# Kernel optimization log

Hardware: AMD Instinct MI355X
Metric: run time of the kernel (lower is better)

Reference implementation:

```python
import jax, jax.numpy as jnp
import numpy as np

N_NODES = 50000
N_EDGES = 800000
IN_CH = 128
OUT_CH = 64
HEADS = 4
NEG_SLOPE = 0.2


def setup_inputs() -> dict:
    key = jax.random.key(0)
    k1, k2, k3, k4, k5 = jax.random.split(key, 5)
    x = jax.random.normal(k1, (N_NODES, IN_CH), dtype=jnp.float32)
    edge_index = jax.random.randint(k2, (2, N_EDGES), 0, N_NODES, dtype=jnp.int64)
    # Glorot-ish scaled params
    W = jax.random.normal(k3, (IN_CH, HEADS * OUT_CH), dtype=jnp.float32) * (1.0 / np.sqrt(IN_CH))
    att_src = jax.random.normal(k4, (HEADS, OUT_CH), dtype=jnp.float32) * (1.0 / np.sqrt(OUT_CH))
    att_dst = jax.random.normal(k5, (HEADS, OUT_CH), dtype=jnp.float32) * (1.0 / np.sqrt(OUT_CH))
    bias = jnp.zeros((HEADS * OUT_CH,), dtype=jnp.float32)
    return {"x": x, "edge_index": edge_index, "W": W, "att_src": att_src, "att_dst": att_dst, "bias": bias}


def reference(x, edge_index, W, att_src, att_dst, bias):
    N = x.shape[0]
    H, C = att_src.shape
    # PyG GATConv default add_self_loops=True
    loops = jnp.arange(N, dtype=edge_index.dtype)
    src = jnp.concatenate([edge_index[0], loops])  # message source j
    dst = jnp.concatenate([edge_index[1], loops])  # message target i
    # Linear transform per head: [N, H, C]
    h = (x @ W).reshape(N, H, C)
    # Per-node attention logits: [N, H]
    a_src = jnp.sum(h * att_src[None], axis=-1)
    a_dst = jnp.sum(h * att_dst[None], axis=-1)
    # Per-edge raw score (alpha_src from source node, alpha_dst from target node)
    e = jax.nn.leaky_relu(a_src[src] + a_dst[dst], NEG_SLOPE)  # [E, H]
    # Segment-softmax over incoming edges of each target node
    m = jax.ops.segment_max(e, dst, num_segments=N)  # [N, H]
    m = jnp.where(jnp.isfinite(m), m, 0.0)  # nodes with no edges -> 0
    ex = jnp.exp(e - m[dst])
    denom = jax.ops.segment_sum(ex, dst, num_segments=N)  # [N, H]
    alpha = ex / (denom[dst] + 1e-16)  # [E, H]
    # Weighted aggregate of source features: [N, H, C]
    msg = h[src] * alpha[:, :, None]
    out = jax.ops.segment_sum(msg, dst, num_segments=N)
    # concat=True: flatten heads, add bias
    return out.reshape(N, H * C) + bias
```

## Files before the change

### kernel.cpp

```cpp
#include <hip/hip_runtime.h>

#define N_NODES 50000
#define N_EDGES 800000
#define IN_CH 128
#define OUT_CH 64
#define HEADS 4
#define HC 256
#define NEG_SLOPE 0.2f
#define GEMM_BLOCKS 782
#define COUNT_BLOCKS 782

#define HB_OFF       0UL
#define WSW_OFF      25600000UL
#define ASRC_OFF     25665536UL
#define ADST_OFF     26465536UL
#define COUNTS_OFF   27265536UL
#define OFFSETS_OFF  27465536UL
#define CURSOR_OFF   27665536UL
#define BSUMS_OFF    27865536UL
#define CSR_OFF      27866560UL
#define EXV_OFF      31066560UL

typedef __attribute__((ext_vector_type(8))) short short8;
typedef __attribute__((ext_vector_type(4))) float f32x4;

__device__ __forceinline__ unsigned short f2bf(float f) {
  unsigned int u = __float_as_uint(f);
  unsigned int r = (u + 0x7fffu + ((u >> 16) & 1u)) >> 16;
  return (unsigned short)r;
}
__device__ __forceinline__ float bf2f_lo(unsigned int u) {
  return __uint_as_float(u << 16);
}
__device__ __forceinline__ float bf2f_hi(unsigned int u) {
  return __uint_as_float(u & 0xffff0000u);
}
__device__ __forceinline__ float lrelu(float e) {
  return e > 0.f ? e : NEG_SLOPE * e;
}

__global__ __launch_bounds__(256) void swizzle_W(const float* __restrict__ W,
                                                 unsigned short* __restrict__ Wsw) {
  int idx = blockIdx.x * 256 + threadIdx.x;
  if (idx >= 4096) return;
  int l = idx & 63;
  int kc = (idx >> 6) & 3;
  int t = idx >> 8;
  int kbase = kc * 32 + (l >> 4) * 8;
  int col = t * 16 + (l & 15);
  unsigned int p[4];
#pragma unroll
  for (int j = 0; j < 4; ++j) {
    unsigned int lo = f2bf(W[(size_t)(kbase + 2 * j) * HC + col]);
    unsigned int hi = f2bf(W[(size_t)(kbase + 2 * j + 1) * HC + col]);
    p[j] = lo | (hi << 16);
  }
  *(uint4*)(Wsw + (size_t)idx * 8) = make_uint4(p[0], p[1], p[2], p[3]);
}

__global__ __launch_bounds__(256) void gemm_count(const float* __restrict__ x,
                                                  const unsigned short* __restrict__ Wsw,
                                                  const float* __restrict__ att_s,
                                                  const float* __restrict__ att_d,
                                                  const int* __restrict__ dstv,
                                                  unsigned short* __restrict__ hb,
                                                  float* __restrict__ a_src,
                                                  float* __restrict__ a_dst,
                                                  int* __restrict__ counts) {
  __shared__ float Cs[4][16][256];

  if (blockIdx.x >= GEMM_BLOCKS) {
    int base = (blockIdx.x - GEMM_BLOCKS) * 1024 + threadIdx.x;
#pragma unroll
    for (int k = 0; k < 4; ++k) {
      int e = base + k * 256;
      if (e < N_EDGES) atomicAdd(&counts[dstv[e]], 1);
    }
    return;
  }

  const int wave = threadIdx.x >> 6;
  const int l = threadIdx.x & 63;
  const int q = l >> 4;
  const int m = l & 15;
  const int mrow = blockIdx.x * 64 + wave * 16 + m;
  const bool mvalid = mrow < N_NODES;
  const int rc = mvalid ? mrow : (N_NODES - 1);

  short8 a[4];
  const float* xr = x + (size_t)rc * IN_CH + q * 8;
#pragma unroll
  for (int kc = 0; kc < 4; ++kc) {
    float4 u = *(const float4*)(xr + kc * 32);
    float4 v = *(const float4*)(xr + kc * 32 + 4);
    short8 t;
    t[0] = (short)f2bf(u.x); t[1] = (short)f2bf(u.y);
    t[2] = (short)f2bf(u.z); t[3] = (short)f2bf(u.w);
    t[4] = (short)f2bf(v.x); t[5] = (short)f2bf(v.y);
    t[6] = (short)f2bf(v.z); t[7] = (short)f2bf(v.w);
    a[kc] = t;
  }

#pragma unroll
  for (int t = 0; t < 16; ++t) {
    f32x4 acc = {0.f, 0.f, 0.f, 0.f};
#pragma unroll
    for (int kc = 0; kc < 4; ++kc) {
      short8 b = *(const short8*)(Wsw + ((size_t)(t * 4 + kc) * 64 + l) * 8);
      acc = __builtin_amdgcn_mfma_f32_16x16x32_bf16(a[kc], b, acc, 0, 0, 0);
    }
#pragma unroll
    for (int r = 0; r < 4; ++r) {
      int row = q * 4 + r;
      Cs[wave][row][(t * 16 + m) ^ (row << 2)] = acc[r];
    }
  }
  __syncthreads();

  float as = 0.f, ad = 0.f;
  unsigned short* hrow = hb + (size_t)mrow * HC + q * 64;
  const int sw = m << 2;
#pragma unroll
  for (int i = 0; i < 8; ++i) {
    int col0 = q * 64 + i * 8;
    float4 c1 = *(const float4*)&Cs[wave][m][(col0) ^ sw];
    float4 c2 = *(const float4*)&Cs[wave][m][(col0 + 4) ^ sw];
    float4 s1 = *(const float4*)(att_s + col0);
    float4 s2 = *(const float4*)(att_s + col0 + 4);
    float4 d1 = *(const float4*)(att_d + col0);
    float4 d2 = *(const float4*)(att_d + col0 + 4);
    as += c1.x * s1.x + c1.y * s1.y + c1.z * s1.z + c1.w * s1.w;
    as += c2.x * s2.x + c2.y * s2.y + c2.z * s2.z + c2.w * s2.w;
    ad += c1.x * d1.x + c1.y * d1.y + c1.z * d1.z + c1.w * d1.w;
    ad += c2.x * d2.x + c2.y * d2.y + c2.z * d2.z + c2.w * d2.w;
    if (mvalid) {
      uint4 p;
      p.x = (unsigned int)f2bf(c1.x) | ((unsigned int)f2bf(c1.y) << 16);
      p.y = (unsigned int)f2bf(c1.z) | ((unsigned int)f2bf(c1.w) << 16);
      p.z = (unsigned int)f2bf(c2.x) | ((unsigned int)f2bf(c2.y) << 16);
      p.w = (unsigned int)f2bf(c2.z) | ((unsigned int)f2bf(c2.w) << 16);
      *(uint4*)(hrow + i * 8) = p;
    }
  }
  if (mvalid) {
    a_src[mrow * HEADS + q] = as;
    a_dst[mrow * HEADS + q] = ad;
  }
}

__global__ __launch_bounds__(256) void scan1(const int* __restrict__ counts,
                                             int* __restrict__ offsets,
                                             int* __restrict__ bsums) {
  __shared__ int sd[256];
  const int base = blockIdx.x * 1024;
  const int t = threadIdx.x;
  int v[4];
  int tsum = 0;
#pragma unroll
  for (int k = 0; k < 4; ++k) {
    int i = base + t * 4 + k;
    v[k] = (i < N_NODES) ? counts[i] : 0;
    tsum += v[k];
  }
  sd[t] = tsum;
  __syncthreads();
  for (int off = 1; off < 256; off <<= 1) {
    int xval = (t >= off) ? sd[t - off] : 0;
    __syncthreads();
    sd[t] += xval;
    __syncthreads();
  }
  int excl = sd[t] - tsum;
  int run = excl;
#pragma unroll
  for (int k = 0; k < 4; ++k) {
    int i = base + t * 4 + k;
    if (i < N_NODES) offsets[i] = run;
    run += v[k];
  }
  if (t == 255) bsums[blockIdx.x] = sd[255];
}

__global__ void scan2(int* __restrict__ bsums, int nb) {
  if (threadIdx.x == 0 && blockIdx.x == 0) {
    int run = 0;
    for (int b = 0; b < nb; ++b) {
      int t = bsums[b];
      bsums[b] = run;
      run += t;
    }
  }
}

__global__ __launch_bounds__(256) void scan3(int* __restrict__ offsets,
                                             const int* __restrict__ bsums,
                                             int* __restrict__ cursor) {
  const int base = blockIdx.x * 1024;
  const int t = threadIdx.x;
  int add = bsums[blockIdx.x];
#pragma unroll
  for (int k = 0; k < 4; ++k) {
    int i = base + t * 4 + k;
    if (i < N_NODES) {
      int o = offsets[i] + add;
      offsets[i] = o;
      cursor[i] = o;
    }
  }
}

__global__ __launch_bounds__(256) void scatter_k(const int* __restrict__ src,
                                                 const int* __restrict__ dst,
                                                 const float* __restrict__ a_src,
                                                 const float* __restrict__ a_dst,
                                                 int* __restrict__ cursor,
                                                 int* __restrict__ csr,
                                                 float* __restrict__ exv) {
  int e = blockIdx.x * 256 + threadIdx.x;
  if (e < N_EDGES) {
    int s = src[e];
    int d = dst[e];
    float4 as = *(const float4*)(a_src + s * 4);
    float4 ad = *(const float4*)(a_dst + d * 4);
    float4 ex;
    ex.x = __expf(lrelu(as.x + ad.x));
    ex.y = __expf(lrelu(as.y + ad.y));
    ex.z = __expf(lrelu(as.z + ad.z));
    ex.w = __expf(lrelu(as.w + ad.w));
    int pos = atomicAdd(&cursor[d], 1);
    csr[pos] = s;
    *(float4*)(exv + (size_t)pos * 4) = ex;
  }
}

__global__ __launch_bounds__(256) void aggregate(const unsigned short* __restrict__ hb,
                                                 const float* __restrict__ a_src,
                                                 const float* __restrict__ a_dst,
                                                 const int* __restrict__ counts,
                                                 const int* __restrict__ offsets,
                                                 const int* __restrict__ csr,
                                                 const float* __restrict__ exv,
                                                 const float* __restrict__ bias,
                                                 float* __restrict__ out) {
  const int node = blockIdx.x * 4 + (threadIdx.x >> 6);
  const int l = threadIdx.x & 63;
  const int g = l >> 5;
  const int q = l & 31;
  const int hd = q >> 3;
  const int c0 = q * 8;
  const int deg = counts[node];
  const int start = offsets[node];

  float denom = 0.f;
  float acc[8] = {0.f, 0.f, 0.f, 0.f, 0.f, 0.f, 0.f, 0.f};
#pragma unroll 2
  for (int j = 0; j + g < deg; j += 2) {
    int idx = start + j + g;
    int s = csr[idx];
    float ex = exv[(size_t)idx * 4 + hd];
    uint4 hv = *(const uint4*)(hb + (size_t)s * HC + c0);
    denom += ex;
    acc[0] += bf2f_lo(hv.x) * ex;
    acc[1] += bf2f_hi(hv.x) * ex;
    acc[2] += bf2f_lo(hv.y) * ex;
    acc[3] += bf2f_hi(hv.y) * ex;
    acc[4] += bf2f_lo(hv.z) * ex;
    acc[5] += bf2f_hi(hv.z) * ex;
    acc[6] += bf2f_lo(hv.w) * ex;
    acc[7] += bf2f_hi(hv.w) * ex;
  }
  denom += __shfl_xor(denom, 32);
#pragma unroll
  for (int k = 0; k < 8; ++k) acc[k] += __shfl_xor(acc[k], 32);

  float es = a_src[node * HEADS + hd] + a_dst[node * HEADS + hd];
  float ex_self = __expf(lrelu(es));
  denom += ex_self;
  uint4 hs = *(const uint4*)(hb + (size_t)node * HC + c0);
  acc[0] += bf2f_lo(hs.x) * ex_self;
  acc[1] += bf2f_hi(hs.x) * ex_self;
  acc[2] += bf2f_lo(hs.y) * ex_self;
  acc[3] += bf2f_hi(hs.y) * ex_self;
  acc[4] += bf2f_lo(hs.z) * ex_self;
  acc[5] += bf2f_hi(hs.z) * ex_self;
  acc[6] += bf2f_lo(hs.w) * ex_self;
  acc[7] += bf2f_hi(hs.w) * ex_self;

  if (g == 0) {
    float inv = 1.f / (denom + 1e-16f);
    float4 b1 = *(const float4*)(bias + c0);
    float4 b2 = *(const float4*)(bias + c0 + 4);
    float4 o1 = make_float4(acc[0] * inv + b1.x, acc[1] * inv + b1.y,
                            acc[2] * inv + b1.z, acc[3] * inv + b1.w);
    float4 o2 = make_float4(acc[4] * inv + b2.x, acc[5] * inv + b2.y,
                            acc[6] * inv + b2.z, acc[7] * inv + b2.w);
    *(float4*)(out + (size_t)node * HC + c0) = o1;
    *(float4*)(out + (size_t)node * HC + c0 + 4) = o2;
  }
}

extern "C" void kernel_launch(void* const* d_in, const int* in_sizes, int n_in,
                              void* d_out, int out_size, void* d_ws, size_t ws_size,
                              hipStream_t stream) {
  const float* x     = (const float*)d_in[0];
  const int*   ei    = (const int*)d_in[1];
  const float* W     = (const float*)d_in[2];
  const float* att_s = (const float*)d_in[3];
  const float* att_d = (const float*)d_in[4];
  const float* bias  = (const float*)d_in[5];
  float* out = (float*)d_out;

  char* ws = (char*)d_ws;
  unsigned short* hb  = (unsigned short*)(ws + HB_OFF);
  unsigned short* Wsw = (unsigned short*)(ws + WSW_OFF);
  float* a_src  = (float*)(ws + ASRC_OFF);
  float* a_dst  = (float*)(ws + ADST_OFF);
  int* counts   = (int*)(ws + COUNTS_OFF);
  int* offsets  = (int*)(ws + OFFSETS_OFF);
  int* cursor   = (int*)(ws + CURSOR_OFF);
  int* bsums    = (int*)(ws + BSUMS_OFF);
  int* csr      = (int*)(ws + CSR_OFF);
  float* exv    = (float*)(ws + EXV_OFF);

  const int* src = ei;
  const int* dst = ei + N_EDGES;

  hipMemsetAsync(counts, 0, N_NODES * sizeof(int), stream);

  swizzle_W<<<16, 256, 0, stream>>>(W, Wsw);
  gemm_count<<<GEMM_BLOCKS + COUNT_BLOCKS, 256, 0, stream>>>(
      x, Wsw, att_s, att_d, dst, hb, a_src, a_dst, counts);
  scan1<<<49, 256, 0, stream>>>(counts, offsets, bsums);
  scan2<<<1, 64, 0, stream>>>(bsums, 49);
  scan3<<<49, 256, 0, stream>>>(offsets, bsums, cursor);
  scatter_k<<<3125, 256, 0, stream>>>(src, dst, a_src, a_dst, cursor, csr, exv);
  aggregate<<<12500, 256, 0, stream>>>(hb, a_src, a_dst, counts, offsets, csr, exv, bias, out);
}
```

Measured before the change: 263.6 us.

## Fuse setup kernels, pack CSR records, widen aggregate to 4 edge groups

The memset is folded into the W swizzle kernel, and scan2/scan3 are merged into one kernel that scans the block sums with a wavefront. This removes two launches. The separate csr and exv arrays become a single 32-byte record per edge holding the source index and the four exp values. The aggregate kernel now processes 4 edges in parallel per wavefront, with each lane covering 16 channels, and a two-step shuffle reduction feeds a store from every lane. The aims are fewer launches, better memory coalescing, and more gather parallelism, at the cost of more registers and padded record traffic.

```diff
diff --git a/kernel.cpp b/kernel.cpp
--- a/kernel.cpp
+++ b/kernel.cpp
@@ -9,6 +9,7 @@
 #define NEG_SLOPE 0.2f
 #define GEMM_BLOCKS 782
 #define COUNT_BLOCKS 782
+#define SCAN_BLOCKS 49
 
 #define HB_OFF       0UL
 #define WSW_OFF      25600000UL
@@ -18,8 +19,7 @@
 #define OFFSETS_OFF  27465536UL
 #define CURSOR_OFF   27665536UL
 #define BSUMS_OFF    27865536UL
-#define CSR_OFF      27866560UL
-#define EXV_OFF      31066560UL
+#define REC_OFF      27866560UL
 
 typedef __attribute__((ext_vector_type(8))) short short8;
 typedef __attribute__((ext_vector_type(4))) float f32x4;
@@ -39,23 +39,28 @@
   return e > 0.f ? e : NEG_SLOPE * e;
 }
 
-__global__ __launch_bounds__(256) void swizzle_W(const float* __restrict__ W,
-                                                 unsigned short* __restrict__ Wsw) {
-  int idx = blockIdx.x * 256 + threadIdx.x;
-  if (idx >= 4096) return;
-  int l = idx & 63;
-  int kc = (idx >> 6) & 3;
-  int t = idx >> 8;
-  int kbase = kc * 32 + (l >> 4) * 8;
-  int col = t * 16 + (l & 15);
-  unsigned int p[4];
-#pragma unroll
-  for (int j = 0; j < 4; ++j) {
-    unsigned int lo = f2bf(W[(size_t)(kbase + 2 * j) * HC + col]);
-    unsigned int hi = f2bf(W[(size_t)(kbase + 2 * j + 1) * HC + col]);
-    p[j] = lo | (hi << 16);
-  }
-  *(uint4*)(Wsw + (size_t)idx * 8) = make_uint4(p[0], p[1], p[2], p[3]);
+__global__ __launch_bounds__(256) void init_k(const float* __restrict__ W,
+                                              unsigned short* __restrict__ Wsw,
+                                              int* __restrict__ counts) {
+  if (blockIdx.x < 16) {
+    int idx = blockIdx.x * 256 + threadIdx.x;
+    int l = idx & 63;
+    int kc = (idx >> 6) & 3;
+    int t = idx >> 8;
+    int kbase = kc * 32 + (l >> 4) * 8;
+    int col = t * 16 + (l & 15);
+    unsigned int p[4];
+#pragma unroll
+    for (int j = 0; j < 4; ++j) {
+      unsigned int lo = f2bf(W[(size_t)(kbase + 2 * j) * HC + col]);
+      unsigned int hi = f2bf(W[(size_t)(kbase + 2 * j + 1) * HC + col]);
+      p[j] = lo | (hi << 16);
+    }
+    *(uint4*)(Wsw + (size_t)idx * 8) = make_uint4(p[0], p[1], p[2], p[3]);
+  } else {
+    int i = (blockIdx.x - 16) * 256 + threadIdx.x;
+    if (i < N_NODES) counts[i] = 0;
+  }
 }
 
 __global__ __launch_bounds__(256) void gemm_count(const float* __restrict__ x,
@@ -181,23 +186,26 @@
   if (t == 255) bsums[blockIdx.x] = sd[255];
 }
 
-__global__ void scan2(int* __restrict__ bsums, int nb) {
-  if (threadIdx.x == 0 && blockIdx.x == 0) {
-    int run = 0;
-    for (int b = 0; b < nb; ++b) {
-      int t = bsums[b];
-      bsums[b] = run;
-      run += t;
-    }
-  }
-}
-
-__global__ __launch_bounds__(256) void scan3(int* __restrict__ offsets,
-                                             const int* __restrict__ bsums,
-                                             int* __restrict__ cursor) {
+__global__ __launch_bounds__(256) void scan23(int* __restrict__ offsets,
+                                              const int* __restrict__ bsums,
+                                              int* __restrict__ cursor) {
+  __shared__ int s_add;
+  if (threadIdx.x < 64) {
+    int lane = threadIdx.x;
+    int v = (lane < SCAN_BLOCKS) ? bsums[lane] : 0;
+#pragma unroll
+    for (int o = 1; o < 64; o <<= 1) {
+      int t = __shfl_up(v, o);
+      if (lane >= o) v += t;
+    }
+    int b = blockIdx.x;
+    int pre = (b == 0) ? 0 : __shfl(v, b - 1);
+    if (lane == 0) s_add = pre;
+  }
+  __syncthreads();
+  const int add = s_add;
   const int base = blockIdx.x * 1024;
   const int t = threadIdx.x;
-  int add = bsums[blockIdx.x];
 #pragma unroll
   for (int k = 0; k < 4; ++k) {
     int i = base + t * 4 + k;
@@ -214,8 +222,7 @@
                                                  const float* __restrict__ a_src,
                                                  const float* __restrict__ a_dst,
                                                  int* __restrict__ cursor,
-                                                 int* __restrict__ csr,
-                                                 float* __restrict__ exv) {
+                                                 char* __restrict__ rec) {
   int e = blockIdx.x * 256 + threadIdx.x;
   if (e < N_EDGES) {
     int s = src[e];
@@ -228,8 +235,10 @@
     ex.z = __expf(lrelu(as.z + ad.z));
     ex.w = __expf(lrelu(as.w + ad.w));
     int pos = atomicAdd(&cursor[d], 1);
-    csr[pos] = s;
-    *(float4*)(exv + (size_t)pos * 4) = ex;
+    char* rp = rec + (size_t)pos * 32;
+    *(uint4*)rp = make_uint4((unsigned)s, __float_as_uint(ex.x),
+                             __float_as_uint(ex.y), __float_as_uint(ex.z));
+    *(unsigned*)(rp + 16) = __float_as_uint(ex.w);
   }
 }
 
@@ -238,65 +247,73 @@
                                                  const float* __restrict__ a_dst,
                                                  const int* __restrict__ counts,
                                                  const int* __restrict__ offsets,
-                                                 const int* __restrict__ csr,
-                                                 const float* __restrict__ exv,
+                                                 const char* __restrict__ rec,
                                                  const float* __restrict__ bias,
                                                  float* __restrict__ out) {
   const int node = blockIdx.x * 4 + (threadIdx.x >> 6);
   const int l = threadIdx.x & 63;
-  const int g = l >> 5;
-  const int q = l & 31;
-  const int hd = q >> 3;
-  const int c0 = q * 8;
+  const int g = l >> 4;
+  const int q = l & 15;
+  const int hd = q >> 2;
+  const int cb = q * 32;
   const int deg = counts[node];
   const int start = offsets[node];
+  const char* hbase = (const char*)hb;
 
   float denom = 0.f;
-  float acc[8] = {0.f, 0.f, 0.f, 0.f, 0.f, 0.f, 0.f, 0.f};
+  float acc[16];
+#pragma unroll
+  for (int k = 0; k < 16; ++k) acc[k] = 0.f;
+
 #pragma unroll 2
-  for (int j = 0; j + g < deg; j += 2) {
+  for (int j = 0; j + g < deg; j += 4) {
     int idx = start + j + g;
-    int s = csr[idx];
-    float ex = exv[(size_t)idx * 4 + hd];
-    uint4 hv = *(const uint4*)(hb + (size_t)s * HC + c0);
+    const char* rp = rec + (size_t)idx * 32;
+    int s = *(const int*)rp;
+    float ex = *(const float*)(rp + 4 + hd * 4);
+    const char* hp = hbase + (size_t)s * 512 + cb;
+    uint4 h0 = *(const uint4*)hp;
+    uint4 h1 = *(const uint4*)(hp + 16);
     denom += ex;
-    acc[0] += bf2f_lo(hv.x) * ex;
-    acc[1] += bf2f_hi(hv.x) * ex;
-    acc[2] += bf2f_lo(hv.y) * ex;
-    acc[3] += bf2f_hi(hv.y) * ex;
-    acc[4] += bf2f_lo(hv.z) * ex;
-    acc[5] += bf2f_hi(hv.z) * ex;
-    acc[6] += bf2f_lo(hv.w) * ex;
-    acc[7] += bf2f_hi(hv.w) * ex;
-  }
+    acc[0] += bf2f_lo(h0.x) * ex;  acc[1] += bf2f_hi(h0.x) * ex;
+    acc[2] += bf2f_lo(h0.y) * ex;  acc[3] += bf2f_hi(h0.y) * ex;
+    acc[4] += bf2f_lo(h0.z) * ex;  acc[5] += bf2f_hi(h0.z) * ex;
+    acc[6] += bf2f_lo(h0.w) * ex;  acc[7] += bf2f_hi(h0.w) * ex;
+    acc[8] += bf2f_lo(h1.x) * ex;  acc[9] += bf2f_hi(h1.x) * ex;
+    acc[10] += bf2f_lo(h1.y) * ex; acc[11] += bf2f_hi(h1.y) * ex;
+    acc[12] += bf2f_lo(h1.z) * ex; acc[13] += bf2f_hi(h1.z) * ex;
+    acc[14] += bf2f_lo(h1.w) * ex; acc[15] += bf2f_hi(h1.w) * ex;
+  }
+
+  denom += __shfl_xor(denom, 16);
   denom += __shfl_xor(denom, 32);
 #pragma unroll
-  for (int k = 0; k < 8; ++k) acc[k] += __shfl_xor(acc[k], 32);
+  for (int k = 0; k < 16; ++k) {
+    acc[k] += __shfl_xor(acc[k], 16);
+    acc[k] += __shfl_xor(acc[k], 32);
+  }
 
   float es = a_src[node * HEADS + hd] + a_dst[node * HEADS + hd];
-  float ex_self = __expf(lrelu(es));
-  denom += ex_self;
-  uint4 hs = *(const uint4*)(hb + (size_t)node * HC + c0);
-  acc[0] += bf2f_lo(hs.x) * ex_self;
-  acc[1] += bf2f_hi(hs.x) * ex_self;
-  acc[2] += bf2f_lo(hs.y) * ex_self;
-  acc[3] += bf2f_hi(hs.y) * ex_self;
-  acc[4] += bf2f_lo(hs.z) * ex_self;
-  acc[5] += bf2f_hi(hs.z) * ex_self;
-  acc[6] += bf2f_lo(hs.w) * ex_self;
-  acc[7] += bf2f_hi(hs.w) * ex_self;
-
-  if (g == 0) {
-    float inv = 1.f / (denom + 1e-16f);
-    float4 b1 = *(const float4*)(bias + c0);
-    float4 b2 = *(const float4*)(bias + c0 + 4);
-    float4 o1 = make_float4(acc[0] * inv + b1.x, acc[1] * inv + b1.y,
-                            acc[2] * inv + b1.z, acc[3] * inv + b1.w);
-    float4 o2 = make_float4(acc[4] * inv + b2.x, acc[5] * inv + b2.y,
-                            acc[6] * inv + b2.z, acc[7] * inv + b2.w);
-    *(float4*)(out + (size_t)node * HC + c0) = o1;
-    *(float4*)(out + (size_t)node * HC + c0 + 4) = o2;
-  }
+  float exs = __expf(lrelu(es));
+  denom += exs;
+  const char* hp = hbase + (size_t)node * 512 + cb;
+  uint4 h0 = *(const uint4*)hp;
+  uint4 h1 = *(const uint4*)(hp + 16);
+  acc[0] += bf2f_lo(h0.x) * exs;  acc[1] += bf2f_hi(h0.x) * exs;
+  acc[2] += bf2f_lo(h0.y) * exs;  acc[3] += bf2f_hi(h0.y) * exs;
+  acc[4] += bf2f_lo(h0.z) * exs;  acc[5] += bf2f_hi(h0.z) * exs;
+  acc[6] += bf2f_lo(h0.w) * exs;  acc[7] += bf2f_hi(h0.w) * exs;
+  acc[8] += bf2f_lo(h1.x) * exs;  acc[9] += bf2f_hi(h1.x) * exs;
+  acc[10] += bf2f_lo(h1.y) * exs; acc[11] += bf2f_hi(h1.y) * exs;
+  acc[12] += bf2f_lo(h1.z) * exs; acc[13] += bf2f_hi(h1.z) * exs;
+  acc[14] += bf2f_lo(h1.w) * exs; acc[15] += bf2f_hi(h1.w) * exs;
+
+  float inv = 1.f / (denom + 1e-16f);
+  int c = q * 16 + g * 4;
+  float4 bv = *(const float4*)(bias + c);
+  float4 o = make_float4(acc[g * 4 + 0] * inv + bv.x, acc[g * 4 + 1] * inv + bv.y,
+                         acc[g * 4 + 2] * inv + bv.z, acc[g * 4 + 3] * inv + bv.w);
+  *(float4*)(out + (size_t)node * HC + c) = o;
 }
 
 extern "C" void kernel_launch(void* const* d_in, const int* in_sizes, int n_in,
@@ -319,20 +336,16 @@
   int* offsets  = (int*)(ws + OFFSETS_OFF);
   int* cursor   = (int*)(ws + CURSOR_OFF);
   int* bsums    = (int*)(ws + BSUMS_OFF);
-  int* csr      = (int*)(ws + CSR_OFF);
-  float* exv    = (float*)(ws + EXV_OFF);
+  char* rec     = (char*)(ws + REC_OFF);
 
   const int* src = ei;
   const int* dst = ei + N_EDGES;
 
-  hipMemsetAsync(counts, 0, N_NODES * sizeof(int), stream);
-
-  swizzle_W<<<16, 256, 0, stream>>>(W, Wsw);
+  init_k<<<16 + 196, 256, 0, stream>>>(W, Wsw, counts);
   gemm_count<<<GEMM_BLOCKS + COUNT_BLOCKS, 256, 0, stream>>>(
       x, Wsw, att_s, att_d, dst, hb, a_src, a_dst, counts);
-  scan1<<<49, 256, 0, stream>>>(counts, offsets, bsums);
-  scan2<<<1, 64, 0, stream>>>(bsums, 49);
-  scan3<<<49, 256, 0, stream>>>(offsets, bsums, cursor);
-  scatter_k<<<3125, 256, 0, stream>>>(src, dst, a_src, a_dst, cursor, csr, exv);
-  aggregate<<<12500, 256, 0, stream>>>(hb, a_src, a_dst, counts, offsets, csr, exv, bias, out);
-}
+  scan1<<<SCAN_BLOCKS, 256, 0, stream>>>(counts, offsets, bsums);
+  scan23<<<SCAN_BLOCKS, 256, 0, stream>>>(offsets, bsums, cursor);
+  scatter_k<<<3125, 256, 0, stream>>>(src, dst, a_src, a_dst, cursor, rec);
+  aggregate<<<12500, 256, 0, stream>>>(hb, a_src, a_dst, counts, offsets, rec, bias, out);
+}
```

Result: faster. 248.7 us (-5.6%).

## Fold attention vectors into W, fuse GEMM with scatter, pack edge records

Applied to the files above, without the earlier changes.

Attention logits are now computed straight from x using precomputed W·att vectors, so the GEMM no longer has to produce them. That lets the bf16 GEMM run in the same launch as the edge scatter, with LDS halved by processing columns in two chunks. The separate memset, swizzle and scan2 launches are merged into an init kernel and a fused scan23. CSR indices and exp weights are packed into 32-byte records so the aggregate reads one record per edge, and its unroll goes from 2 to 4. The trade-off is a second read of x and logits computed in fp32 from the folded weights, which differ slightly from the bf16-derived values.

```diff
diff --git a/kernel.cpp b/kernel.cpp
--- a/kernel.cpp
+++ b/kernel.cpp
@@ -7,8 +7,11 @@
 #define HEADS 4
 #define HC 256
 #define NEG_SLOPE 0.2f
+#define LOGIT_BLOCKS 3125
+#define CNT_BLOCKS 782
 #define GEMM_BLOCKS 782
-#define COUNT_BLOCKS 782
+#define SCAT_BLOCKS 3125
+#define SCAN_BLOCKS 49
 
 #define HB_OFF       0UL
 #define WSW_OFF      25600000UL
@@ -18,8 +21,9 @@
 #define OFFSETS_OFF  27465536UL
 #define CURSOR_OFF   27665536UL
 #define BSUMS_OFF    27865536UL
-#define CSR_OFF      27866560UL
-#define EXV_OFF      31066560UL
+#define WSV_OFF      27866560UL
+#define WDV_OFF      27868608UL
+#define REC_OFF      27870656UL
 
 typedef __attribute__((ext_vector_type(8))) short short8;
 typedef __attribute__((ext_vector_type(4))) float f32x4;
@@ -39,43 +43,185 @@
   return e > 0.f ? e : NEG_SLOPE * e;
 }
 
-__global__ __launch_bounds__(256) void swizzle_W(const float* __restrict__ W,
-                                                 unsigned short* __restrict__ Wsw) {
-  int idx = blockIdx.x * 256 + threadIdx.x;
-  if (idx >= 4096) return;
-  int l = idx & 63;
-  int kc = (idx >> 6) & 3;
-  int t = idx >> 8;
-  int kbase = kc * 32 + (l >> 4) * 8;
-  int col = t * 16 + (l & 15);
-  unsigned int p[4];
-#pragma unroll
-  for (int j = 0; j < 4; ++j) {
-    unsigned int lo = f2bf(W[(size_t)(kbase + 2 * j) * HC + col]);
-    unsigned int hi = f2bf(W[(size_t)(kbase + 2 * j + 1) * HC + col]);
-    p[j] = lo | (hi << 16);
-  }
-  *(uint4*)(Wsw + (size_t)idx * 8) = make_uint4(p[0], p[1], p[2], p[3]);
-}
-
-__global__ __launch_bounds__(256) void gemm_count(const float* __restrict__ x,
-                                                  const unsigned short* __restrict__ Wsw,
-                                                  const float* __restrict__ att_s,
-                                                  const float* __restrict__ att_d,
-                                                  const int* __restrict__ dstv,
-                                                  unsigned short* __restrict__ hb,
-                                                  float* __restrict__ a_src,
-                                                  float* __restrict__ a_dst,
-                                                  int* __restrict__ counts) {
-  __shared__ float Cs[4][16][256];
-
-  if (blockIdx.x >= GEMM_BLOCKS) {
-    int base = (blockIdx.x - GEMM_BLOCKS) * 1024 + threadIdx.x;
+__global__ __launch_bounds__(256) void init_k(const float* __restrict__ W,
+                                              const float* __restrict__ att_s,
+                                              const float* __restrict__ att_d,
+                                              unsigned short* __restrict__ Wsw,
+                                              float* __restrict__ wsv,
+                                              float* __restrict__ wdv,
+                                              int* __restrict__ counts) {
+  if (blockIdx.x < 16) {
+    int idx = blockIdx.x * 256 + threadIdx.x;
+    int l = idx & 63;
+    int kc = (idx >> 6) & 3;
+    int t = idx >> 8;
+    int kbase = kc * 32 + (l >> 4) * 8;
+    int col = t * 16 + (l & 15);
+    unsigned int p[4];
+#pragma unroll
+    for (int j = 0; j < 4; ++j) {
+      unsigned int lo = f2bf(W[(size_t)(kbase + 2 * j) * HC + col]);
+      unsigned int hi = f2bf(W[(size_t)(kbase + 2 * j + 1) * HC + col]);
+      p[j] = lo | (hi << 16);
+    }
+    *(uint4*)(Wsw + (size_t)idx * 8) = make_uint4(p[0], p[1], p[2], p[3]);
+  } else if (blockIdx.x == 16) {
+    int t = threadIdx.x;
+    int k = t >> 1;
+    int side = t & 1;
+    const float* att = side ? att_d : att_s;
+    float v[4] = {0.f, 0.f, 0.f, 0.f};
+    const float* wr = W + (size_t)k * HC;
+    for (int c = 0; c < 64; ++c) {
+#pragma unroll
+      for (int hd = 0; hd < 4; ++hd) v[hd] = fmaf(wr[hd * 64 + c], att[hd * 64 + c], v[hd]);
+    }
+    float* dp = side ? wdv : wsv;
+    *(float4*)(dp + k * 4) = make_float4(v[0], v[1], v[2], v[3]);
+  } else {
+    int i = (blockIdx.x - 17) * 256 + threadIdx.x;
+    if (i < N_NODES) counts[i] = 0;
+  }
+}
+
+__global__ __launch_bounds__(256) void logits_count(const float* __restrict__ x,
+                                                    const float* __restrict__ wsv,
+                                                    const float* __restrict__ wdv,
+                                                    const int* __restrict__ dstv,
+                                                    float* __restrict__ a_src,
+                                                    float* __restrict__ a_dst,
+                                                    int* __restrict__ counts) {
+  if (blockIdx.x >= LOGIT_BLOCKS) {
+    int base = (blockIdx.x - LOGIT_BLOCKS) * 1024 + threadIdx.x;
 #pragma unroll
     for (int k = 0; k < 4; ++k) {
       int e = base + k * 256;
       if (e < N_EDGES) atomicAdd(&counts[dstv[e]], 1);
     }
+    return;
+  }
+  const int t = threadIdx.x;
+  const int nl = t >> 4;
+  const int lane = t & 15;
+  const int node = blockIdx.x * 16 + nl;
+  const float* xr = x + (size_t)node * IN_CH + lane * 8;
+  float4 x0 = *(const float4*)xr;
+  float4 x1 = *(const float4*)(xr + 4);
+  float xs[8] = {x0.x, x0.y, x0.z, x0.w, x1.x, x1.y, x1.z, x1.w};
+  float as[4] = {0.f, 0.f, 0.f, 0.f}, ad[4] = {0.f, 0.f, 0.f, 0.f};
+#pragma unroll
+  for (int j = 0; j < 8; ++j) {
+    int k = lane * 8 + j;
+    float4 wv = *(const float4*)(wsv + k * 4);
+    float4 dv = *(const float4*)(wdv + k * 4);
+    as[0] = fmaf(xs[j], wv.x, as[0]); as[1] = fmaf(xs[j], wv.y, as[1]);
+    as[2] = fmaf(xs[j], wv.z, as[2]); as[3] = fmaf(xs[j], wv.w, as[3]);
+    ad[0] = fmaf(xs[j], dv.x, ad[0]); ad[1] = fmaf(xs[j], dv.y, ad[1]);
+    ad[2] = fmaf(xs[j], dv.z, ad[2]); ad[3] = fmaf(xs[j], dv.w, ad[3]);
+  }
+#pragma unroll
+  for (int mask = 1; mask < 16; mask <<= 1) {
+#pragma unroll
+    for (int hd = 0; hd < 4; ++hd) {
+      as[hd] += __shfl_xor(as[hd], mask);
+      ad[hd] += __shfl_xor(ad[hd], mask);
+    }
+  }
+  if (lane == 0) *(float4*)(a_src + node * 4) = make_float4(as[0], as[1], as[2], as[3]);
+  if (lane == 1) *(float4*)(a_dst + node * 4) = make_float4(ad[0], ad[1], ad[2], ad[3]);
+}
+
+__global__ __launch_bounds__(256) void scan1(const int* __restrict__ counts,
+                                             int* __restrict__ offsets,
+                                             int* __restrict__ bsums) {
+  __shared__ int sd[256];
+  const int base = blockIdx.x * 1024;
+  const int t = threadIdx.x;
+  int v[4];
+  int tsum = 0;
+#pragma unroll
+  for (int k = 0; k < 4; ++k) {
+    int i = base + t * 4 + k;
+    v[k] = (i < N_NODES) ? counts[i] : 0;
+    tsum += v[k];
+  }
+  sd[t] = tsum;
+  __syncthreads();
+  for (int off = 1; off < 256; off <<= 1) {
+    int xval = (t >= off) ? sd[t - off] : 0;
+    __syncthreads();
+    sd[t] += xval;
+    __syncthreads();
+  }
+  int excl = sd[t] - tsum;
+  int run = excl;
+#pragma unroll
+  for (int k = 0; k < 4; ++k) {
+    int i = base + t * 4 + k;
+    if (i < N_NODES) offsets[i] = run;
+    run += v[k];
+  }
+  if (t == 255) bsums[blockIdx.x] = sd[255];
+}
+
+__global__ __launch_bounds__(256) void scan23(int* __restrict__ offsets,
+                                              const int* __restrict__ bsums,
+                                              int* __restrict__ cursor) {
+  __shared__ int s_add;
+  if (threadIdx.x < 64) {
+    int lane = threadIdx.x;
+    int v = (lane < SCAN_BLOCKS) ? bsums[lane] : 0;
+#pragma unroll
+    for (int o = 1; o < 64; o <<= 1) {
+      int t = __shfl_up(v, o);
+      if (lane >= o) v += t;
+    }
+    int b = blockIdx.x;
+    int pre = (b == 0) ? 0 : __shfl(v, b - 1);
+    if (lane == 0) s_add = pre;
+  }
+  __syncthreads();
+  const int add = s_add;
+  const int base = blockIdx.x * 1024;
+  const int t = threadIdx.x;
+#pragma unroll
+  for (int k = 0; k < 4; ++k) {
+    int i = base + t * 4 + k;
+    if (i < N_NODES) {
+      int o = offsets[i] + add;
+      offsets[i] = o;
+      cursor[i] = o;
+    }
+  }
+}
+
+__global__ __launch_bounds__(256) void gemm_scatter(const float* __restrict__ x,
+                                                    const unsigned short* __restrict__ Wsw,
+                                                    const int* __restrict__ srcv,
+                                                    const int* __restrict__ dstv,
+                                                    const float* __restrict__ a_src,
+                                                    const float* __restrict__ a_dst,
+                                                    int* __restrict__ cursor,
+                                                    char* __restrict__ rec,
+                                                    unsigned short* __restrict__ hb) {
+  __shared__ float Cs[4][16][128];
+
+  if (blockIdx.x >= GEMM_BLOCKS) {
+    int e = (blockIdx.x - GEMM_BLOCKS) * 256 + threadIdx.x;
+    int s = srcv[e];
+    int d = dstv[e];
+    float4 as = *(const float4*)(a_src + s * 4);
+    float4 ad = *(const float4*)(a_dst + d * 4);
+    float4 ex;
+    ex.x = __expf(lrelu(as.x + ad.x));
+    ex.y = __expf(lrelu(as.y + ad.y));
+    ex.z = __expf(lrelu(as.z + ad.z));
+    ex.w = __expf(lrelu(as.w + ad.w));
+    int pos = atomicAdd(&cursor[d], 1);
+    char* rp = rec + (size_t)pos * 32;
+    *(uint4*)rp = make_uint4((unsigned)s, __float_as_uint(ex.x),
+                             __float_as_uint(ex.y), __float_as_uint(ex.z));
+    *(unsigned*)(rp + 16) = __float_as_uint(ex.w);
     return;
   }
 
@@ -101,135 +247,40 @@
     a[kc] = t;
   }
 
-#pragma unroll
-  for (int t = 0; t < 16; ++t) {
-    f32x4 acc = {0.f, 0.f, 0.f, 0.f};
-#pragma unroll
-    for (int kc = 0; kc < 4; ++kc) {
-      short8 b = *(const short8*)(Wsw + ((size_t)(t * 4 + kc) * 64 + l) * 8);
-      acc = __builtin_amdgcn_mfma_f32_16x16x32_bf16(a[kc], b, acc, 0, 0, 0);
-    }
-#pragma unroll
-    for (int r = 0; r < 4; ++r) {
-      int row = q * 4 + r;
-      Cs[wave][row][(t * 16 + m) ^ (row << 2)] = acc[r];
-    }
-  }
-  __syncthreads();
-
-  float as = 0.f, ad = 0.f;
   unsigned short* hrow = hb + (size_t)mrow * HC + q * 64;
   const int sw = m << 2;
 #pragma unroll
-  for (int i = 0; i < 8; ++i) {
-    int col0 = q * 64 + i * 8;
-    float4 c1 = *(const float4*)&Cs[wave][m][(col0) ^ sw];
-    float4 c2 = *(const float4*)&Cs[wave][m][(col0 + 4) ^ sw];
-    float4 s1 = *(const float4*)(att_s + col0);
-    float4 s2 = *(const float4*)(att_s + col0 + 4);
-    float4 d1 = *(const float4*)(att_d + col0);
-    float4 d2 = *(const float4*)(att_d + col0 + 4);
-    as += c1.x * s1.x + c1.y * s1.y + c1.z * s1.z + c1.w * s1.w;
-    as += c2.x * s2.x + c2.y * s2.y + c2.z * s2.z + c2.w * s2.w;
-    ad += c1.x * d1.x + c1.y * d1.y + c1.z * d1.z + c1.w * d1.w;
-    ad += c2.x * d2.x + c2.y * d2.y + c2.z * d2.z + c2.w * d2.w;
-    if (mvalid) {
-      uint4 p;
-      p.x = (unsigned int)f2bf(c1.x) | ((unsigned int)f2bf(c1.y) << 16);
-      p.y = (unsigned int)f2bf(c1.z) | ((unsigned int)f2bf(c1.w) << 16);
-      p.z = (unsigned int)f2bf(c2.x) | ((unsigned int)f2bf(c2.y) << 16);
-      p.w = (unsigned int)f2bf(c2.z) | ((unsigned int)f2bf(c2.w) << 16);
-      *(uint4*)(hrow + i * 8) = p;
-    }
-  }
-  if (mvalid) {
-    a_src[mrow * HEADS + q] = as;
-    a_dst[mrow * HEADS + q] = ad;
-  }
-}
-
-__global__ __launch_bounds__(256) void scan1(const int* __restrict__ counts,
-                                             int* __restrict__ offsets,
-                                             int* __restrict__ bsums) {
-  __shared__ int sd[256];
-  const int base = blockIdx.x * 1024;
-  const int t = threadIdx.x;
-  int v[4];
-  int tsum = 0;
-#pragma unroll
-  for (int k = 0; k < 4; ++k) {
-    int i = base + t * 4 + k;
-    v[k] = (i < N_NODES) ? counts[i] : 0;
-    tsum += v[k];
-  }
-  sd[t] = tsum;
-  __syncthreads();
-  for (int off = 1; off < 256; off <<= 1) {
-    int xval = (t >= off) ? sd[t - off] : 0;
-    __syncthreads();
-    sd[t] += xval;
-    __syncthreads();
-  }
-  int excl = sd[t] - tsum;
-  int run = excl;
-#pragma unroll
-  for (int k = 0; k < 4; ++k) {
-    int i = base + t * 4 + k;
-    if (i < N_NODES) offsets[i] = run;
-    run += v[k];
-  }
-  if (t == 255) bsums[blockIdx.x] = sd[255];
-}
-
-__global__ void scan2(int* __restrict__ bsums, int nb) {
-  if (threadIdx.x == 0 && blockIdx.x == 0) {
-    int run = 0;
-    for (int b = 0; b < nb; ++b) {
-      int t = bsums[b];
-      bsums[b] = run;
-      run += t;
-    }
-  }
-}
-
-__global__ __launch_bounds__(256) void scan3(int* __restrict__ offsets,
-                                             const int* __restrict__ bsums,
-                                             int* __restrict__ cursor) {
-  const int base = blockIdx.x * 1024;
-  const int t = threadIdx.x;
-  int add = bsums[blockIdx.x];
-#pragma unroll
-  for (int k = 0; k < 4; ++k) {
-    int i = base + t * 4 + k;
-    if (i < N_NODES) {
-      int o = offsets[i] + add;
-      offsets[i] = o;
-      cursor[i] = o;
-    }
-  }
-}
-
-__global__ __launch_bounds__(256) void scatter_k(const int* __restrict__ src,
-                                                 const int* __restrict__ dst,
-                                                 const float* __restrict__ a_src,
-                                                 const float* __restrict__ a_dst,
-                                                 int* __restrict__ cursor,
-                                                 int* __restrict__ csr,
-                                                 float* __restrict__ exv) {
-  int e = blockIdx.x * 256 + threadIdx.x;
-  if (e < N_EDGES) {
-    int s = src[e];
-    int d = dst[e];
-    float4 as = *(const float4*)(a_src + s * 4);
-    float4 ad = *(const float4*)(a_dst + d * 4);
-    float4 ex;
-    ex.x = __expf(lrelu(as.x + ad.x));
-    ex.y = __expf(lrelu(as.y + ad.y));
-    ex.z = __expf(lrelu(as.z + ad.z));
-    ex.w = __expf(lrelu(as.w + ad.w));
-    int pos = atomicAdd(&cursor[d], 1);
-    csr[pos] = s;
-    *(float4*)(exv + (size_t)pos * 4) = ex;
+  for (int chunk = 0; chunk < 2; ++chunk) {
+#pragma unroll
+    for (int t8 = 0; t8 < 8; ++t8) {
+      const int t = chunk * 8 + t8;
+      f32x4 acc = {0.f, 0.f, 0.f, 0.f};
+#pragma unroll
+      for (int kc = 0; kc < 4; ++kc) {
+        short8 b = *(const short8*)(Wsw + ((size_t)(t * 4 + kc) * 64 + l) * 8);
+        acc = __builtin_amdgcn_mfma_f32_16x16x32_bf16(a[kc], b, acc, 0, 0, 0);
+      }
+#pragma unroll
+      for (int r = 0; r < 4; ++r) {
+        int row = q * 4 + r;
+        Cs[wave][row][(t8 * 16 + m) ^ (row << 2)] = acc[r];
+      }
+    }
+    if ((q >> 1) == chunk && mvalid) {
+      const int cb = (q & 1) * 64;
+#pragma unroll
+      for (int i = 0; i < 8; ++i) {
+        int c0 = cb + i * 8;
+        float4 c1 = *(const float4*)&Cs[wave][m][(c0) ^ sw];
+        float4 c2 = *(const float4*)&Cs[wave][m][(c0 + 4) ^ sw];
+        uint4 p;
+        p.x = (unsigned int)f2bf(c1.x) | ((unsigned int)f2bf(c1.y) << 16);
+        p.y = (unsigned int)f2bf(c1.z) | ((unsigned int)f2bf(c1.w) << 16);
+        p.z = (unsigned int)f2bf(c2.x) | ((unsigned int)f2bf(c2.y) << 16);
+        p.w = (unsigned int)f2bf(c2.z) | ((unsigned int)f2bf(c2.w) << 16);
+        *(uint4*)(hrow + i * 8) = p;
+      }
+    }
   }
 }
 
@@ -238,8 +289,7 @@
                                                  const float* __restrict__ a_dst,
                                                  const int* __restrict__ counts,
                                                  const int* __restrict__ offsets,
-                                                 const int* __restrict__ csr,
-                                                 const float* __restrict__ exv,
+                                                 const char* __restrict__ rec,
                                                  const float* __restrict__ bias,
                                                  float* __restrict__ out) {
   const int node = blockIdx.x * 4 + (threadIdx.x >> 6);
@@ -253,11 +303,12 @@
 
   float denom = 0.f;
   float acc[8] = {0.f, 0.f, 0.f, 0.f, 0.f, 0.f, 0.f, 0.f};
-#pragma unroll 2
+#pragma unroll 4
   for (int j = 0; j + g < deg; j += 2) {
     int idx = start + j + g;
-    int s = csr[idx];
-    float ex = exv[(size_t)idx * 4 + hd];
+    const char* rp = rec + (size_t)idx * 32;
+    int s = *(const int*)rp;
+    float ex = *(const float*)(rp + 4 + hd * 4);
     uint4 hv = *(const uint4*)(hb + (size_t)s * HC + c0);
     denom += ex;
     acc[0] += bf2f_lo(hv.x) * ex;
@@ -319,20 +370,19 @@
   int* offsets  = (int*)(ws + OFFSETS_OFF);
   int* cursor   = (int*)(ws + CURSOR_OFF);
   int* bsums    = (int*)(ws + BSUMS_OFF);
-  int* csr      = (int*)(ws + CSR_OFF);
-  float* exv    = (float*)(ws + EXV_OFF);
+  float* wsv    = (float*)(ws + WSV_OFF);
+  float* wdv    = (float*)(ws + WDV_OFF);
+  char* rec     = (char*)(ws + REC_OFF);
 
   const int* src = ei;
   const int* dst = ei + N_EDGES;
 
-  hipMemsetAsync(counts, 0, N_NODES * sizeof(int), stream);
-
-  swizzle_W<<<16, 256, 0, stream>>>(W, Wsw);
-  gemm_count<<<GEMM_BLOCKS + COUNT_BLOCKS, 256, 0, stream>>>(
-      x, Wsw, att_s, att_d, dst, hb, a_src, a_dst, counts);
-  scan1<<<49, 256, 0, stream>>>(counts, offsets, bsums);
-  scan2<<<1, 64, 0, stream>>>(bsums, 49);
-  scan3<<<49, 256, 0, stream>>>(offsets, bsums, cursor);
-  scatter_k<<<3125, 256, 0, stream>>>(src, dst, a_src, a_dst, cursor, csr, exv);
-  aggregate<<<12500, 256, 0, stream>>>(hb, a_src, a_dst, counts, offsets, csr, exv, bias, out);
-}
+  init_k<<<17 + 196, 256, 0, stream>>>(W, att_s, att_d, Wsw, wsv, wdv, counts);
+  logits_count<<<LOGIT_BLOCKS + CNT_BLOCKS, 256, 0, stream>>>(
+      x, wsv, wdv, dst, a_src, a_dst, counts);
+  scan1<<<SCAN_BLOCKS, 256, 0, stream>>>(counts, offsets, bsums);
+  scan23<<<SCAN_BLOCKS, 256, 0, stream>>>(offsets, bsums, cursor);
+  gemm_scatter<<<GEMM_BLOCKS + SCAT_BLOCKS, 256, 0, stream>>>(
+      x, Wsw, src, dst, a_src, a_dst, cursor, rec, hb);
+  aggregate<<<12500, 256, 0, stream>>>(hb, a_src, a_dst, counts, offsets, rec, bias, out);
+}
```

Result: slower. 279.1 us (+5.9%).
